# Kernel optimization log

Hardware: AMD Instinct MI355X
Metric: run time of the kernel (lower is better)

Reference implementation:

```python
import jax, jax.numpy as jnp
import numpy as np

B, H, W = 8, 512, 1024
ALPHA = BETA = GAMMA = DELTA = 1.0
MASK_COST = 12.4


def _sig(x, t, mu=1.0):
    return jax.nn.sigmoid(mu * (x - t))


def _penalty(x):
    return jnp.sqrt(x + 1e-5)


def _border_mask(flow):
    b, _, h, w = flow.shape
    X = jnp.arange(w, dtype=flow.dtype)[None, None, :] + flow[:, 0]
    Y = jnp.arange(h, dtype=flow.dtype)[None, :, None] + flow[:, 1]
    mx = _sig(X, -0.5) * (1.0 - _sig(X, w - 0.5))
    my = _sig(Y, -0.5) * (1.0 - _sig(Y, h - 0.5))
    return mx * my


def _warp(src, flow):
    # bilinear resample of src (B,C,H,W) at x+flow_x, y+flow_y with border-clamped indices
    b, c, h, w = src.shape
    gx = jnp.arange(w, dtype=src.dtype)[None, None, :] + flow[:, 0]
    gy = jnp.arange(h, dtype=src.dtype)[None, :, None] + flow[:, 1]
    x0 = jnp.floor(gx)
    y0 = jnp.floor(gy)
    ax = (gx - x0)[..., None]
    ay = (gy - y0)[..., None]
    x0i = jnp.clip(x0.astype(jnp.int32), 0, w - 1)
    x1i = jnp.clip(x0.astype(jnp.int32) + 1, 0, w - 1)
    y0i = jnp.clip(y0.astype(jnp.int32), 0, h - 1)
    y1i = jnp.clip(y0.astype(jnp.int32) + 1, 0, h - 1)
    s = jnp.transpose(src, (0, 2, 3, 1))  # BHWC
    bi = jnp.arange(b)[:, None, None]
    v00 = s[bi, y0i, x0i]
    v01 = s[bi, y0i, x1i]
    v10 = s[bi, y1i, x0i]
    v11 = s[bi, y1i, x1i]
    out = (1 - ay) * ((1 - ax) * v00 + ax * v01) + ay * ((1 - ax) * v10 + ax * v11)
    return jnp.transpose(out, (0, 3, 1, 2))


def _grad5(x, horizontal):
    # depthwise cross-correlation with taps [-1/12, 2/3, 0, -2/3, 1/12], zero pad 2
    taps = (-1.0 / 12, 2.0 / 3, 0.0, -2.0 / 3, 1.0 / 12)
    if horizontal:
        xp = jnp.pad(x, ((0, 0), (0, 0), (0, 0), (2, 2)))
        n = x.shape[3]
        return sum(taps[k] * xp[:, :, :, k:k + n] for k in (0, 1, 3, 4))
    else:
        xp = jnp.pad(x, ((0, 0), (0, 0), (2, 2), (0, 0)))
        n = x.shape[2]
        return sum(taps[k] * xp[:, :, k:k + n, :] for k in (0, 1, 3, 4))


def _smooth_term(flow):
    dx = flow[:, :, :, 1:] - flow[:, :, :, :-1]
    dy = flow[:, :, 1:, :] - flow[:, :, :-1, :]
    Bm = (jnp.pad(jnp.sum(dx ** 2, axis=1), ((0, 0), (0, 0), (0, 1)))
          + jnp.pad(jnp.sum(dy ** 2, axis=1), ((0, 0), (0, 1), (0, 0))))
    return jnp.sum(_penalty(Bm), axis=(1, 2))


def _dir_terms(flowa, flowb, imga, imgb):
    mask = _border_mask(flowa)
    flowb_w = _warp(flowb, flowa)
    mag = jnp.sum(flowa ** 2 + flowb_w ** 2, axis=1)
    d2 = jnp.sum((flowa + flowb_w) ** 2, axis=1)
    occ = 1.0 - _sig(d2, 0.01 * mag + 0.5)
    mask = mask * occ
    mask_term = jnp.sum(1.0 - mask, axis=(1, 2))
    imgb_w = _warp(imgb, flowa)
    A = jnp.sum((imga - imgb_w) ** 2, axis=1)
    data_term = jnp.sum(_penalty(A) * mask, axis=(1, 2))
    smooth_term = _smooth_term(flowa)
    C = (jnp.sum((_grad5(imga, True) - _grad5(imgb_w, True)) ** 2, axis=1)
         + jnp.sum((_grad5(imga, False) - _grad5(imgb_w, False)) ** 2, axis=1))
    grad_term = jnp.sum(_penalty(C) * mask, axis=(1, 2))
    return data_term, smooth_term, grad_term, mask_term, mask, d2


def setup_inputs() -> dict:
    key = jax.random.key(0)
    k1, k2, k3, k4, k5 = jax.random.split(key, 5)
    flowf = 3.0 * jax.random.normal(k1, (B, 2, H, W), dtype=jnp.float32)
    flowb = 3.0 * jax.random.normal(k2, (B, 2, H, W), dtype=jnp.float32)
    img1 = jax.random.uniform(k3, (B, 3, H, W), dtype=jnp.float32)
    img2 = jax.random.uniform(k4, (B, 3, H, W), dtype=jnp.float32)
    target = 3.0 * jax.random.normal(k5, (B, 2, H, W), dtype=jnp.float32)
    return {"flowf": flowf, "flowb": flowb, "img1": img1, "img2": img2, "target": target}


def reference(flowf, flowb, img1, img2, target):
    df, sf, gf, mf, maskf, Df = _dir_terms(flowf, flowb, img1, img2)
    db, sb, gb, mb, maskb, Db = _dir_terms(flowb, flowf, img2, img1)
    fb = jnp.sum(_penalty(Df) * maskf + _penalty(Db) * maskb, axis=(1, 2))
    energy = (ALPHA * (df + db) + BETA * (sf + sb) + GAMMA * (gf + gb)
              + MASK_COST * (mf + mb) + DELTA * fb)
    epe = jnp.mean(jnp.sqrt(jnp.sum((flowf - target) ** 2, axis=1)))
    return jnp.stack([jnp.mean(energy), epe])
```

## Files before the change

### kernel.cpp

```cpp
#include <hip/hip_runtime.h>

#define BB 8
#define HH 512
#define WW 1024
#define TILE 32
#define HALO 2
#define LW (TILE + 2*HALO)

__device__ __forceinline__ float sigm(float v) { return 1.0f / (1.0f + __expf(-v)); }

template<int C>
__device__ __forceinline__ void bilin(const float* __restrict__ src, int b,
                                      float gx, float gy, float out[C]) {
    float x0f = floorf(gx), y0f = floorf(gy);
    float ax = gx - x0f, ay = gy - y0f;
    int x0 = (int)x0f, y0 = (int)y0f;
    int x0i = min(max(x0, 0), WW - 1);
    int x1i = min(max(x0 + 1, 0), WW - 1);
    int y0i = min(max(y0, 0), HH - 1);
    int y1i = min(max(y0 + 1, 0), HH - 1);
    float w00 = (1.f - ay) * (1.f - ax), w01 = (1.f - ay) * ax;
    float w10 = ay * (1.f - ax), w11 = ay * ax;
#pragma unroll
    for (int c = 0; c < C; ++c) {
        const float* p = src + (size_t)(b * C + c) * (HH * WW);
        float v00 = p[y0i * WW + x0i];
        float v01 = p[y0i * WW + x1i];
        float v10 = p[y1i * WW + x0i];
        float v11 = p[y1i * WW + x1i];
        out[c] = w00 * v00 + w01 * v01 + w10 * v10 + w11 * v11;
    }
}

template<bool EPE>
__global__ __launch_bounds__(256)
void dir_kernel(const float* __restrict__ flowa, const float* __restrict__ flowb,
                const float* __restrict__ imga, const float* __restrict__ imgb,
                const float* __restrict__ target, float* __restrict__ acc) {
    __shared__ float lds_w[3][LW][LW];
    __shared__ float lds_a[3][LW][LW];
    __shared__ float red[8];

    const int b = blockIdx.z;
    const int tx0 = blockIdx.x * TILE;
    const int ty0 = blockIdx.y * TILE;
    const int tid = threadIdx.x;
    const size_t plane = (size_t)HH * WW;

    for (int p = tid; p < LW * LW; p += 256) {
        int hy = p / LW, hx = p % LW;
        int gy = ty0 + hy - HALO, gx = tx0 + hx - HALO;
        float w[3] = {0.f, 0.f, 0.f};
        float a0 = 0.f, a1 = 0.f, a2 = 0.f;
        if (gx >= 0 && gx < WW && gy >= 0 && gy < HH) {
            size_t fi = (size_t)(b * 2) * plane + (size_t)gy * WW + gx;
            float fx = flowa[fi];
            float fy = flowa[fi + plane];
            bilin<3>(imgb, b, (float)gx + fx, (float)gy + fy, w);
            size_t ii = (size_t)(b * 3) * plane + (size_t)gy * WW + gx;
            a0 = imga[ii];
            a1 = imga[ii + plane];
            a2 = imga[ii + 2 * plane];
        }
        lds_w[0][hy][hx] = w[0]; lds_w[1][hy][hx] = w[1]; lds_w[2][hy][hx] = w[2];
        lds_a[0][hy][hx] = a0;   lds_a[1][hy][hx] = a1;   lds_a[2][hy][hx] = a2;
    }
    __syncthreads();

    float local = 0.f, lepe = 0.f;
    const float T0 = 1.f / 12.f, T1 = 2.f / 3.f;

#pragma unroll
    for (int i = 0; i < 4; ++i) {
        int p = i * 256 + tid;
        int ly = p >> 5, lx = p & 31;
        int y = ty0 + ly, x = tx0 + lx;

        size_t fi = (size_t)(b * 2) * plane + (size_t)y * WW + x;
        float fx = flowa[fi], fy = flowa[fi + plane];
        float X = (float)x + fx, Y = (float)y + fy;

        float mask = sigm(X + 0.5f) * (1.f - sigm(X - ((float)WW - 0.5f)))
                   * sigm(Y + 0.5f) * (1.f - sigm(Y - ((float)HH - 0.5f)));

        float wf[2];
        bilin<2>(flowb, b, X, Y, wf);
        float mag = fx * fx + fy * fy + wf[0] * wf[0] + wf[1] * wf[1];
        float sx = fx + wf[0], sy = fy + wf[1];
        float d2 = sx * sx + sy * sy;
        float occ = 1.f - sigm(d2 - (0.01f * mag + 0.5f));
        mask *= occ;

        float A = 0.f;
#pragma unroll
        for (int c = 0; c < 3; ++c) {
            float d = lds_a[c][ly + 2][lx + 2] - lds_w[c][ly + 2][lx + 2];
            A += d * d;
        }

        float sm = 0.f;
        if (x < WW - 1) {
            float dfx = flowa[fi + 1] - fx;
            float dfy = flowa[fi + plane + 1] - fy;
            sm += dfx * dfx + dfy * dfy;
        }
        if (y < HH - 1) {
            float dfx = flowa[fi + WW] - fx;
            float dfy = flowa[fi + plane + WW] - fy;
            sm += dfx * dfx + dfy * dfy;
        }

        float C = 0.f;
#pragma unroll
        for (int c = 0; c < 3; ++c) {
            float gha = T1 * (lds_a[c][ly + 2][lx + 1] - lds_a[c][ly + 2][lx + 3])
                      + T0 * (lds_a[c][ly + 2][lx + 4] - lds_a[c][ly + 2][lx]);
            float ghw = T1 * (lds_w[c][ly + 2][lx + 1] - lds_w[c][ly + 2][lx + 3])
                      + T0 * (lds_w[c][ly + 2][lx + 4] - lds_w[c][ly + 2][lx]);
            float d = gha - ghw;
            C += d * d;
            float gva = T1 * (lds_a[c][ly + 1][lx + 2] - lds_a[c][ly + 3][lx + 2])
                      + T0 * (lds_a[c][ly + 4][lx + 2] - lds_a[c][ly][lx + 2]);
            float gvw = T1 * (lds_w[c][ly + 1][lx + 2] - lds_w[c][ly + 3][lx + 2])
                      + T0 * (lds_w[c][ly + 4][lx + 2] - lds_w[c][ly][lx + 2]);
            d = gva - gvw;
            C += d * d;
        }

        local += sqrtf(A + 1e-5f) * mask
               + sqrtf(sm + 1e-5f)
               + sqrtf(C + 1e-5f) * mask
               + 12.4f * (1.f - mask)
               + sqrtf(d2 + 1e-5f) * mask;

        if (EPE) {
            float dx = fx - target[fi];
            float dy = fy - target[fi + plane];
            lepe += sqrtf(dx * dx + dy * dy);
        }
    }

#pragma unroll
    for (int off = 32; off > 0; off >>= 1) {
        local += __shfl_down(local, off);
        if (EPE) lepe += __shfl_down(lepe, off);
    }
    int wid = tid >> 6;
    if ((tid & 63) == 0) { red[wid] = local; red[4 + wid] = lepe; }
    __syncthreads();
    if (tid == 0) {
        atomicAdd(&acc[0], red[0] + red[1] + red[2] + red[3]);
        if (EPE) atomicAdd(&acc[1], red[4] + red[5] + red[6] + red[7]);
    }
}

__global__ void finalize_kernel(const float* __restrict__ acc, float* __restrict__ out) {
    out[0] = acc[0] / (float)BB;
    out[1] = acc[1] / (float)((size_t)BB * HH * WW);
}

extern "C" void kernel_launch(void* const* d_in, const int* in_sizes, int n_in,
                              void* d_out, int out_size, void* d_ws, size_t ws_size,
                              hipStream_t stream) {
    const float* flowf  = (const float*)d_in[0];
    const float* flowb  = (const float*)d_in[1];
    const float* img1   = (const float*)d_in[2];
    const float* img2   = (const float*)d_in[3];
    const float* target = (const float*)d_in[4];
    float* out = (float*)d_out;
    float* acc = (float*)d_ws;

    hipMemsetAsync(acc, 0, 2 * sizeof(float), stream);

    dim3 grid(WW / TILE, HH / TILE, BB);
    dir_kernel<true ><<<grid, 256, 0, stream>>>(flowf, flowb, img1, img2, target, acc);
    dir_kernel<false><<<grid, 256, 0, stream>>>(flowb, flowf, img2, img1, nullptr, acc);

    finalize_kernel<<<1, 1, 0, stream>>>(acc, out);
}
```

Measured before the change: 364.8 us.

## Merge both directions into one launch and vectorize bilinear gathers

Both flow directions now run in a single launch, with the direction selected from blockIdx.z. Removing the second launch and its tail lets blocks from both directions overlap. Bilinear sampling now loads each horizontal neighbour pair as one float2 per row, with clamped fallbacks at the image edges. The halo flow values are loaded up front into registers so the gathers can be issued with more memory-level parallelism. Launch bounds request 4 blocks per SM, which may raise register pressure; the float2 loads may also be misaligned when x0 is odd, which on HIP is legal but can split into two accesses.

```diff
diff --git a/kernel.cpp b/kernel.cpp
--- a/kernel.cpp
+++ b/kernel.cpp
@@ -6,64 +6,94 @@
 #define TILE 32
 #define HALO 2
 #define LW (TILE + 2*HALO)
+#define NIT ((LW*LW + 255) / 256)
 
 __device__ __forceinline__ float sigm(float v) { return 1.0f / (1.0f + __expf(-v)); }
 
+__device__ __forceinline__ float2 ld2c(const float* __restrict__ row, int x0) {
+    if ((unsigned)x0 < (unsigned)(WW - 1)) {
+        return *reinterpret_cast<const float2*>(row + x0);
+    }
+    float v = row[x0 < 0 ? 0 : WW - 1];
+    return make_float2(v, v);
+}
+
 template<int C>
-__device__ __forceinline__ void bilin(const float* __restrict__ src, int b,
-                                      float gx, float gy, float out[C]) {
+__device__ __forceinline__ void bilinN(const float* __restrict__ base,
+                                       float gx, float gy, float out[C]) {
+    const size_t plane = (size_t)HH * WW;
     float x0f = floorf(gx), y0f = floorf(gy);
     float ax = gx - x0f, ay = gy - y0f;
     int x0 = (int)x0f, y0 = (int)y0f;
-    int x0i = min(max(x0, 0), WW - 1);
-    int x1i = min(max(x0 + 1, 0), WW - 1);
     int y0i = min(max(y0, 0), HH - 1);
     int y1i = min(max(y0 + 1, 0), HH - 1);
     float w00 = (1.f - ay) * (1.f - ax), w01 = (1.f - ay) * ax;
     float w10 = ay * (1.f - ax), w11 = ay * ax;
 #pragma unroll
     for (int c = 0; c < C; ++c) {
-        const float* p = src + (size_t)(b * C + c) * (HH * WW);
-        float v00 = p[y0i * WW + x0i];
-        float v01 = p[y0i * WW + x1i];
-        float v10 = p[y1i * WW + x0i];
-        float v11 = p[y1i * WW + x1i];
-        out[c] = w00 * v00 + w01 * v01 + w10 * v10 + w11 * v11;
-    }
-}
-
-template<bool EPE>
-__global__ __launch_bounds__(256)
-void dir_kernel(const float* __restrict__ flowa, const float* __restrict__ flowb,
-                const float* __restrict__ imga, const float* __restrict__ imgb,
+        const float* pl = base + c * plane;
+        float2 r0 = ld2c(pl + (size_t)y0i * WW, x0);
+        float2 r1 = ld2c(pl + (size_t)y1i * WW, x0);
+        out[c] = w00 * r0.x + w01 * r0.y + w10 * r1.x + w11 * r1.y;
+    }
+}
+
+__global__ __launch_bounds__(256, 4)
+void dir_kernel(const float* __restrict__ flowf, const float* __restrict__ flowb_,
+                const float* __restrict__ img1, const float* __restrict__ img2,
                 const float* __restrict__ target, float* __restrict__ acc) {
     __shared__ float lds_w[3][LW][LW];
     __shared__ float lds_a[3][LW][LW];
     __shared__ float red[8];
 
-    const int b = blockIdx.z;
+    const int z = blockIdx.z;
+    const int dir = z >> 3;
+    const int b = z & 7;
+    const float* flowa = dir ? flowb_ : flowf;
+    const float* flowb = dir ? flowf : flowb_;
+    const float* imga  = dir ? img2 : img1;
+    const float* imgb  = dir ? img1 : img2;
+
     const int tx0 = blockIdx.x * TILE;
     const int ty0 = blockIdx.y * TILE;
     const int tid = threadIdx.x;
     const size_t plane = (size_t)HH * WW;
-
-    for (int p = tid; p < LW * LW; p += 256) {
-        int hy = p / LW, hx = p % LW;
+    const size_t fbase = (size_t)(b * 2) * plane;
+    const size_t ibase = (size_t)(b * 3) * plane;
+
+    float fxs[NIT], fys[NIT];
+#pragma unroll
+    for (int it = 0; it < NIT; ++it) {
+        int p = tid + it * 256;
+        int hy = p / LW, hx = p - hy * LW;
         int gy = ty0 + hy - HALO, gx = tx0 + hx - HALO;
-        float w[3] = {0.f, 0.f, 0.f};
-        float a0 = 0.f, a1 = 0.f, a2 = 0.f;
-        if (gx >= 0 && gx < WW && gy >= 0 && gy < HH) {
-            size_t fi = (size_t)(b * 2) * plane + (size_t)gy * WW + gx;
-            float fx = flowa[fi];
-            float fy = flowa[fi + plane];
-            bilin<3>(imgb, b, (float)gx + fx, (float)gy + fy, w);
-            size_t ii = (size_t)(b * 3) * plane + (size_t)gy * WW + gx;
-            a0 = imga[ii];
-            a1 = imga[ii + plane];
-            a2 = imga[ii + 2 * plane];
-        }
-        lds_w[0][hy][hx] = w[0]; lds_w[1][hy][hx] = w[1]; lds_w[2][hy][hx] = w[2];
-        lds_a[0][hy][hx] = a0;   lds_a[1][hy][hx] = a1;   lds_a[2][hy][hx] = a2;
+        float fx = 0.f, fy = 0.f;
+        if (p < LW * LW && (unsigned)gx < WW && (unsigned)gy < HH) {
+            size_t fi = fbase + (size_t)gy * WW + gx;
+            fx = flowa[fi];
+            fy = flowa[fi + plane];
+        }
+        fxs[it] = fx; fys[it] = fy;
+    }
+
+#pragma unroll
+    for (int it = 0; it < NIT; ++it) {
+        int p = tid + it * 256;
+        if (p < LW * LW) {
+            int hy = p / LW, hx = p - hy * LW;
+            int gy = ty0 + hy - HALO, gx = tx0 + hx - HALO;
+            float w[3] = {0.f, 0.f, 0.f};
+            float a0 = 0.f, a1 = 0.f, a2 = 0.f;
+            if ((unsigned)gx < WW && (unsigned)gy < HH) {
+                bilinN<3>(imgb + ibase, (float)gx + fxs[it], (float)gy + fys[it], w);
+                size_t ii = ibase + (size_t)gy * WW + gx;
+                a0 = imga[ii];
+                a1 = imga[ii + plane];
+                a2 = imga[ii + 2 * plane];
+            }
+            lds_w[0][hy][hx] = w[0]; lds_w[1][hy][hx] = w[1]; lds_w[2][hy][hx] = w[2];
+            lds_a[0][hy][hx] = a0;   lds_a[1][hy][hx] = a1;   lds_a[2][hy][hx] = a2;
+        }
     }
     __syncthreads();
 
@@ -76,7 +106,7 @@
         int ly = p >> 5, lx = p & 31;
         int y = ty0 + ly, x = tx0 + lx;
 
-        size_t fi = (size_t)(b * 2) * plane + (size_t)y * WW + x;
+        size_t fi = fbase + (size_t)y * WW + x;
         float fx = flowa[fi], fy = flowa[fi + plane];
         float X = (float)x + fx, Y = (float)y + fy;
 
@@ -84,7 +114,7 @@
                    * sigm(Y + 0.5f) * (1.f - sigm(Y - ((float)HH - 0.5f)));
 
         float wf[2];
-        bilin<2>(flowb, b, X, Y, wf);
+        bilinN<2>(flowb + fbase, X, Y, wf);
         float mag = fx * fx + fy * fy + wf[0] * wf[0] + wf[1] * wf[1];
         float sx = fx + wf[0], sy = fy + wf[1];
         float d2 = sx * sx + sy * sy;
@@ -133,7 +163,7 @@
                + 12.4f * (1.f - mask)
                + sqrtf(d2 + 1e-5f) * mask;
 
-        if (EPE) {
+        if (dir == 0) {
             float dx = fx - target[fi];
             float dy = fy - target[fi + plane];
             lepe += sqrtf(dx * dx + dy * dy);
@@ -143,14 +173,14 @@
 #pragma unroll
     for (int off = 32; off > 0; off >>= 1) {
         local += __shfl_down(local, off);
-        if (EPE) lepe += __shfl_down(lepe, off);
+        lepe  += __shfl_down(lepe, off);
     }
     int wid = tid >> 6;
     if ((tid & 63) == 0) { red[wid] = local; red[4 + wid] = lepe; }
     __syncthreads();
     if (tid == 0) {
         atomicAdd(&acc[0], red[0] + red[1] + red[2] + red[3]);
-        if (EPE) atomicAdd(&acc[1], red[4] + red[5] + red[6] + red[7]);
+        if (dir == 0) atomicAdd(&acc[1], red[4] + red[5] + red[6] + red[7]);
     }
 }
 
@@ -172,9 +202,8 @@
 
     hipMemsetAsync(acc, 0, 2 * sizeof(float), stream);
 
-    dim3 grid(WW / TILE, HH / TILE, BB);
-    dir_kernel<true ><<<grid, 256, 0, stream>>>(flowf, flowb, img1, img2, target, acc);
-    dir_kernel<false><<<grid, 256, 0, stream>>>(flowb, flowf, img2, img1, nullptr, acc);
+    dim3 grid(WW / TILE, HH / TILE, 2 * BB);
+    dir_kernel<<<grid, 256, 0, stream>>>(flowf, flowb, img1, img2, target, acc);
 
     finalize_kernel<<<1, 1, 0, stream>>>(acc, out);
 }
```

Measured after the change: 930.0 us. +155.0%, slower.
